# Optimization experiments

Measured on AMD Instinct MI355X. Metric: run time of the kernel, lower is better.

## Reference

```python
import jax, jax.numpy as jnp
import numpy as np

B, S, VD, MD = 32, 2048, 512, 512
AD = max(VD, MD)


def setup_inputs() -> dict:
    key = jax.random.key(0)
    k1, k2, k3, k4, k5, k6 = jax.random.split(key, 6)
    query = jax.random.normal(k1, (B, VD), dtype=jnp.float32)
    keys = jax.random.normal(k2, (B, S, MD), dtype=jnp.float32)
    mask = jax.random.randint(k3, (B, S), 0, 2).astype(jnp.bool_)
    # torch Linear weight layout: [out, in]
    W1 = jax.random.normal(k4, (AD, VD), dtype=jnp.float32) * (1.0 / np.sqrt(VD))
    W2 = jax.random.normal(k5, (AD, MD), dtype=jnp.float32) * (1.0 / np.sqrt(MD))
    v = jax.random.normal(k6, (AD,), dtype=jnp.float32) * (1.0 / np.sqrt(AD))
    return {"query": query, "keys": keys, "mask": mask, "W1": W1, "W2": W2, "v": v}


def reference(query, keys, mask, W1, W2, v):
    # w1_query: [B, 1, AD]; w2_keys: [B, S, AD]
    w1_query = jnp.einsum('bd,ad->ba', query, W1)[:, None, :]
    w2_keys = jnp.einsum('bsd,ad->bsa', keys, W2)
    combined = jnp.tanh(w1_query + w2_keys)            # [B, S, AD]
    scores = jnp.einsum('bsa,a->bs', combined, v)      # [B, S]
    scores = jnp.where(mask, scores, -jnp.inf)
    attn_weights = jax.nn.softmax(scores, axis=-1)
    return attn_weights
```

## Files before the change

### kernel.cpp

```cpp
#include <hip/hip_runtime.h>
#include <math.h>

#define BB 32
#define SS 2048
#define DD 512
#define AD 512

#define BM 128
#define BN 128
#define BK 64

typedef __bf16 bf16;
typedef __attribute__((ext_vector_type(8))) __bf16 bf16x8;
typedef __attribute__((ext_vector_type(4))) __bf16 bf16x4;
typedef __attribute__((ext_vector_type(4))) float floatx4;

__device__ inline void async16(const void* g, void* l) {
    __builtin_amdgcn_global_load_lds(
        (const __attribute__((address_space(1))) unsigned int*)g,
        (__attribute__((address_space(3))) unsigned int*)l, 16, 0, 0);
}

#define NW8 (AD * DD / 8)
#define NCV (NW8 / 256)
__global__ void prep_kernel(const float* __restrict__ W2,
                            bf16* __restrict__ W2b,
                            const unsigned char* __restrict__ m8,
                            int* __restrict__ flag,
                            const float* __restrict__ query,
                            const float* __restrict__ W1,
                            float* __restrict__ w1q) {
    const int bid = blockIdx.x;
    if (bid < NCV) {
        int j = threadIdx.x + bid * 256;
        const float4* s4 = (const float4*)W2 + (size_t)j * 2;
        float4 x = s4[0], y = s4[1];
        bf16x8 o;
        o[0] = (bf16)x.x; o[1] = (bf16)x.y; o[2] = (bf16)x.z; o[3] = (bf16)x.w;
        o[4] = (bf16)y.x; o[5] = (bf16)y.y; o[6] = (bf16)y.z; o[7] = (bf16)y.w;
        *(bf16x8*)(W2b + (size_t)j * 8) = o;
    } else if (bid < NCV + 64) {
        int t = threadIdx.x + (bid - NCV) * 256;
        int any = 0;
        for (int i = t; i < BB * SS; i += 64 * 256)
            if ((i & 3) && m8[i]) any = 1;
        if (__any(any)) {
            if ((threadIdx.x & 63) == 0) atomicOr(flag, 1);
        }
    } else {
        int id = bid - NCV - 64;
        int b = id >> 7;
        int a = (id & 127) * 4 + (threadIdx.x >> 6);
        int lane = threadIdx.x & 63;
        const float4* q4 = (const float4*)(query + (size_t)b * DD) + lane * 2;
        const float4* w4 = (const float4*)(W1 + (size_t)a * DD) + lane * 2;
        float4 qa = q4[0], qb = q4[1];
        float4 wa = w4[0], wb = w4[1];
        float acc = qa.x * wa.x + qa.y * wa.y + qa.z * wa.z + qa.w * wa.w
                  + qb.x * wb.x + qb.y * wb.y + qb.z * wb.z + qb.w * wb.w;
#pragma unroll
        for (int off = 32; off > 0; off >>= 1) acc += __shfl_down(acc, off);
        if (lane == 0) w1q[(size_t)b * AD + a] = acc;
    }
}

__global__ __launch_bounds__(256, 3)
void gemm_scores_mfma(const float* __restrict__ keys,
                      const bf16* __restrict__ W2b,
                      const float* __restrict__ w1q,
                      const float* __restrict__ v,
                      float* __restrict__ partial) {
    __shared__ float a_lds[BM * BK];
    __shared__ bf16  b_lds[BN * BK];

    const int t    = threadIdx.x;
    const int lane = t & 63;
    const int w    = t >> 6;
    const int ml   = lane & 15;
    const int kg   = lane >> 4;

    const int lin    = blockIdx.x;
    const int x8     = lin & 7;
    const int hi     = lin >> 3;
    const int a_tile = hi & 3;
    const int kt     = x8 + ((hi >> 2) << 3);
    const int b      = kt >> 4;
    const int s0     = (kt & 15) * BM;
    const int a0     = a_tile * BN;

    const int m_off = (w & 1) * 64;
    const int n_off = (w >> 1) * 64;

    const float* Ablk = keys + ((size_t)b * SS + s0) * DD;
    const bf16*  Bblk = W2b + (size_t)a0 * DD;

    floatx4 acc[4][4];
#pragma unroll
    for (int mi = 0; mi < 4; ++mi)
#pragma unroll
        for (int ni = 0; ni < 4; ++ni)
            acc[mi][ni] = (floatx4)(0.f);

    const int NCHUNK = DD / BK;
    for (int c = 0; c < NCHUNK; ++c) {
        const int d0 = c * BK;
        __syncthreads();
#pragma unroll
        for (int i = 0; i < 8; ++i) {
            int g = t + 256 * i;
            int r = g >> 4, cc = g & 15, cs = cc ^ (r & 15);
            async16(Ablk + (size_t)r * DD + d0 + cs * 4,
                    &a_lds[(256 * i + 64 * w) * 4]);
        }
#pragma unroll
        for (int i = 0; i < 4; ++i) {
            int g = t + 256 * i;
            int r = g >> 3, cc = g & 7, cs = cc ^ (r & 7);
            async16(Bblk + (size_t)r * DD + d0 + cs * 8,
                    &b_lds[(256 * i + 64 * w) * 8]);
        }
        __syncthreads();

#pragma unroll
        for (int ks = 0; ks < 2; ++ks) {
            bf16x8 af[4], bfr[4];
#pragma unroll
            for (int mi = 0; mi < 4; ++mi) {
                int R  = m_off + mi * 16 + ml;
                int gB = 8 * ks + 2 * kg;
                float4 lo = *(const float4*)&a_lds[R * BK + ((gB    ) ^ (R & 15)) * 4];
                float4 hi4 = *(const float4*)&a_lds[R * BK + ((gB + 1) ^ (R & 15)) * 4];
                bf16x8 f;
                f[0] = (bf16)lo.x;  f[1] = (bf16)lo.y;
                f[2] = (bf16)lo.z;  f[3] = (bf16)lo.w;
                f[4] = (bf16)hi4.x; f[5] = (bf16)hi4.y;
                f[6] = (bf16)hi4.z; f[7] = (bf16)hi4.w;
                af[mi] = f;
            }
#pragma unroll
            for (int ni = 0; ni < 4; ++ni) {
                int R = n_off + ni * 16 + ml;
                int pos = (ks * 4 + kg) ^ (R & 7);
                bfr[ni] = *(const bf16x8*)&b_lds[R * BK + pos * 8];
            }
#pragma unroll
            for (int mi = 0; mi < 4; ++mi)
#pragma unroll
                for (int ni = 0; ni < 4; ++ni)
                    acc[mi][ni] = __builtin_amdgcn_mfma_f32_16x16x32_bf16(
                        af[mi], bfr[ni], acc[mi][ni], 0, 0, 0);
        }
    }

    float w1qa[4], va[4];
#pragma unroll
    for (int ni = 0; ni < 4; ++ni) {
        int a = a0 + n_off + ni * 16 + ml;
        w1qa[ni] = w1q[(size_t)b * AD + a];
        va[ni]   = v[a];
    }
    const int slot = a_tile * 2 + (w >> 1);
#pragma unroll
    for (int mi = 0; mi < 4; ++mi) {
#pragma unroll
        for (int reg = 0; reg < 4; ++reg) {
            float p = 0.f;
#pragma unroll
            for (int ni = 0; ni < 4; ++ni) {
                float x = acc[mi][ni][reg] + w1qa[ni];
                float th = 1.f - 2.f / (1.f + __expf(2.f * x));
                p = fmaf(th, va[ni], p);
            }
            p += __shfl_xor(p, 1);
            p += __shfl_xor(p, 2);
            p += __shfl_xor(p, 4);
            p += __shfl_xor(p, 8);
            if (ml == 0) {
                int row = m_off + mi * 16 + kg * 4 + reg;
                partial[((size_t)b * SS + s0 + row) * 8 + slot] = p;
            }
        }
    }
}

#define FBK 32
#define FLDK (FBK + 8)
__global__ __launch_bounds__(256, 2)
void gemm_scores_fallback(const float* __restrict__ keys,
                          const float* __restrict__ W2,
                          const float* __restrict__ w1q,
                          const float* __restrict__ v,
                          float* __restrict__ partial) {
    __shared__ bf16 a_lds[BM][FLDK];
    __shared__ bf16 b_lds[BN][FLDK];
    __shared__ float s_red[BM];

    const int t    = threadIdx.x;
    const int lane = t & 63;
    const int w    = t >> 6;
    const int ml   = lane & 15;
    const int kg   = lane >> 4;
    const int b    = blockIdx.z;
    const int s0   = blockIdx.x * BM;
    const int a0   = blockIdx.y * BN;
    const int m_off = (w & 1) * 64;
    const int n_off = (w >> 1) * 64;

    const float* Ablk = keys + ((size_t)b * SS + s0) * DD;
    const float* Bblk = W2 + (size_t)a0 * DD;

    if (t < BM) s_red[t] = 0.f;

    floatx4 acc[4][4];
#pragma unroll
    for (int mi = 0; mi < 4; ++mi)
#pragma unroll
        for (int ni = 0; ni < 4; ++ni)
            acc[mi][ni] = (floatx4)(0.f);

    float4 ga[4], gb[4];
#pragma unroll
    for (int i = 0; i < 4; ++i) {
        int idx = t + 256 * i;
        int r = idx >> 3, c = idx & 7;
        ga[i] = *(const float4*)(Ablk + (size_t)r * DD + c * 4);
        gb[i] = *(const float4*)(Bblk + (size_t)r * DD + c * 4);
    }

    for (int chunk = 0; chunk < DD / FBK; ++chunk) {
        __syncthreads();
#pragma unroll
        for (int i = 0; i < 4; ++i) {
            int idx = t + 256 * i;
            int r = idx >> 3, c = idx & 7;
            bf16x4 pa, pb;
            pa[0] = (bf16)ga[i].x; pa[1] = (bf16)ga[i].y;
            pa[2] = (bf16)ga[i].z; pa[3] = (bf16)ga[i].w;
            pb[0] = (bf16)gb[i].x; pb[1] = (bf16)gb[i].y;
            pb[2] = (bf16)gb[i].z; pb[3] = (bf16)gb[i].w;
            *(bf16x4*)&a_lds[r][c * 4] = pa;
            *(bf16x4*)&b_lds[r][c * 4] = pb;
        }
        __syncthreads();
        if (chunk < DD / FBK - 1) {
            int d0 = (chunk + 1) * FBK;
#pragma unroll
            for (int i = 0; i < 4; ++i) {
                int idx = t + 256 * i;
                int r = idx >> 3, c = idx & 7;
                ga[i] = *(const float4*)(Ablk + (size_t)r * DD + d0 + c * 4);
                gb[i] = *(const float4*)(Bblk + (size_t)r * DD + d0 + c * 4);
            }
        }
        bf16x8 af[4], bfr[4];
#pragma unroll
        for (int mi = 0; mi < 4; ++mi)
            af[mi] = *(const bf16x8*)&a_lds[m_off + mi * 16 + ml][kg * 8];
#pragma unroll
        for (int ni = 0; ni < 4; ++ni)
            bfr[ni] = *(const bf16x8*)&b_lds[n_off + ni * 16 + ml][kg * 8];
#pragma unroll
        for (int mi = 0; mi < 4; ++mi)
#pragma unroll
            for (int ni = 0; ni < 4; ++ni)
                acc[mi][ni] = __builtin_amdgcn_mfma_f32_16x16x32_bf16(
                    af[mi], bfr[ni], acc[mi][ni], 0, 0, 0);
    }

    float w1qa[4], va[4];
#pragma unroll
    for (int ni = 0; ni < 4; ++ni) {
        int a = a0 + n_off + ni * 16 + ml;
        w1qa[ni] = w1q[(size_t)b * AD + a];
        va[ni]   = v[a];
    }
#pragma unroll
    for (int mi = 0; mi < 4; ++mi) {
#pragma unroll
        for (int reg = 0; reg < 4; ++reg) {
            float p = 0.f;
#pragma unroll
            for (int ni = 0; ni < 4; ++ni) {
                float x = acc[mi][ni][reg] + w1qa[ni];
                float th = 1.f - 2.f / (1.f + __expf(2.f * x));
                p = fmaf(th, va[ni], p);
            }
            p += __shfl_xor(p, 1);
            p += __shfl_xor(p, 2);
            p += __shfl_xor(p, 4);
            p += __shfl_xor(p, 8);
            if (ml == 0)
                atomicAdd(&s_red[m_off + mi * 16 + kg * 4 + reg], p);
        }
    }
    __syncthreads();
    if (t < BM)
        partial[(((size_t)b * SS) + s0 + t) * 8 + blockIdx.y * 2] = s_red[t];
}

__global__ void softmax_kernel(const float* __restrict__ partial,
                               const int* __restrict__ mask_i32,
                               const unsigned char* __restrict__ mask_u8,
                               const int* __restrict__ flag,
                               float* __restrict__ out) {
    const int b = blockIdx.x;
    const int t = threadIdx.x;
    __shared__ float rmax[4], rsum[4];
    const int wid = t >> 6, lane = t & 63;

    float sv[8]; int mv[8];
    const int bytes = (*flag != 0);
#pragma unroll
    for (int k = 0; k < 8; ++k) {
        int i = t + 256 * k;
        const float4* p4 = (const float4*)(partial + ((size_t)b * SS + i) * 8);
        float4 pa = p4[0], pb = p4[1];
        sv[k] = ((pa.x + pa.y) + (pa.z + pa.w)) + ((pb.x + pb.y) + (pb.z + pb.w));
        mv[k] = bytes ? (int)mask_u8[(size_t)b * SS + i]
                      : mask_i32[(size_t)b * SS + i];
    }

    float mx = -INFINITY;
#pragma unroll
    for (int k = 0; k < 8; ++k) mx = fmaxf(mx, mv[k] ? sv[k] : -INFINITY);
#pragma unroll
    for (int off = 32; off > 0; off >>= 1) mx = fmaxf(mx, __shfl_xor(mx, off));
    if (lane == 0) rmax[wid] = mx;
    __syncthreads();
    mx = fmaxf(fmaxf(rmax[0], rmax[1]), fmaxf(rmax[2], rmax[3]));

    float ev[8]; float sum = 0.f;
#pragma unroll
    for (int k = 0; k < 8; ++k) {
        ev[k] = mv[k] ? __expf(sv[k] - mx) : 0.f;
        sum += ev[k];
    }
#pragma unroll
    for (int off = 32; off > 0; off >>= 1) sum += __shfl_xor(sum, off);
    if (lane == 0) rsum[wid] = sum;
    __syncthreads();
    sum = (rsum[0] + rsum[1]) + (rsum[2] + rsum[3]);
    float inv = 1.f / sum;
#pragma unroll
    for (int k = 0; k < 8; ++k)
        out[(size_t)b * SS + t + 256 * k] = ev[k] * inv;
}

extern "C" void kernel_launch(void* const* d_in, const int* in_sizes, int n_in,
                              void* d_out, int out_size, void* d_ws, size_t ws_size,
                              hipStream_t stream) {
    const float* query = (const float*)d_in[0];
    const float* keys  = (const float*)d_in[1];
    const void*  mask  = d_in[2];
    const float* W1    = (const float*)d_in[3];
    const float* W2    = (const float*)d_in[4];
    const float* v     = (const float*)d_in[5];
    float* out = (float*)d_out;

    char* wsb = (char*)d_ws;
    int*   flag    = (int*)wsb;
    float* w1q     = (float*)(wsb + 256);
    float* partial = (float*)(wsb + 256 + 65536);
    bf16*  W2b     = (bf16*)(wsb + 256 + 65536 + 2097152);
    size_t need = 256 + 65536 + 2097152 + (size_t)AD * DD * 2;

    hipMemsetAsync(flag, 0, 4, stream);
    if (ws_size >= need) {
        prep_kernel<<<NCV + 64 + 4096, 256, 0, stream>>>(
            W2, W2b, (const unsigned char*)mask, flag, query, W1, w1q);
        gemm_scores_mfma<<<(SS / BM) * (AD / BN) * BB, 256, 0, stream>>>(
            keys, W2b, w1q, v, partial);
    } else {
        hipMemsetAsync(partial, 0, (size_t)BB * SS * 8 * 4, stream);
        prep_kernel<<<NCV + 64 + 4096, 256, 0, stream>>>(
            W2, W2b, (const unsigned char*)mask, flag, query, W1, w1q);
        gemm_scores_fallback<<<dim3(SS / BM, AD / BN, BB), 256, 0, stream>>>(
            keys, W2, w1q, v, partial);
    }
    softmax_kernel<<<BB, 256, 0, stream>>>(partial, (const int*)mask,
                                           (const unsigned char*)mask, flag, out);
}
```

Measured before the change: 244.2 us.

## Double-buffer LDS staging in scores GEMM with halved K chunk

```diff
diff --git a/kernel.cpp b/kernel.cpp
--- a/kernel.cpp
+++ b/kernel.cpp
@@ -8,7 +8,7 @@
 
 #define BM 128
 #define BN 128
-#define BK 64
+#define BK 32
 
 typedef __bf16 bf16;
 typedef __attribute__((ext_vector_type(8))) __bf16 bf16x8;
@@ -64,14 +64,34 @@
     }
 }
 
+__device__ inline void stage_chunk(const float* __restrict__ Ablk,
+                                   const bf16* __restrict__ Bblk,
+                                   int d0, float* al, bf16* bl,
+                                   int t, int w) {
+#pragma unroll
+    for (int i = 0; i < 4; ++i) {
+        int g = t + 256 * i;
+        int r = g >> 3, cc = g & 7, cs = cc ^ (r & 7);
+        async16(Ablk + (size_t)r * DD + d0 + cs * 4,
+                al + (256 * i + 64 * w) * 4);
+    }
+#pragma unroll
+    for (int i = 0; i < 2; ++i) {
+        int g = t + 256 * i;
+        int r = g >> 2, cc = g & 3, cs = cc ^ (r & 3);
+        async16(Bblk + (size_t)r * DD + d0 + cs * 8,
+                bl + (256 * i + 64 * w) * 8);
+    }
+}
+
 __global__ __launch_bounds__(256, 3)
 void gemm_scores_mfma(const float* __restrict__ keys,
                       const bf16* __restrict__ W2b,
                       const float* __restrict__ w1q,
                       const float* __restrict__ v,
                       float* __restrict__ partial) {
-    __shared__ float a_lds[BM * BK];
-    __shared__ bf16  b_lds[BN * BK];
+    __shared__ float a_lds[2][BM * BK];
+    __shared__ bf16  b_lds[2][BN * BK];
 
     const int t    = threadIdx.x;
     const int lane = t & 63;
@@ -102,54 +122,43 @@
             acc[mi][ni] = (floatx4)(0.f);
 
     const int NCHUNK = DD / BK;
+
+    stage_chunk(Ablk, Bblk, 0, &a_lds[0][0], &b_lds[0][0], t, w);
+
     for (int c = 0; c < NCHUNK; ++c) {
-        const int d0 = c * BK;
+        const int cur = c & 1;
         __syncthreads();
-#pragma unroll
-        for (int i = 0; i < 8; ++i) {
-            int g = t + 256 * i;
-            int r = g >> 4, cc = g & 15, cs = cc ^ (r & 15);
-            async16(Ablk + (size_t)r * DD + d0 + cs * 4,
-                    &a_lds[(256 * i + 64 * w) * 4]);
-        }
-#pragma unroll
-        for (int i = 0; i < 4; ++i) {
-            int g = t + 256 * i;
-            int r = g >> 3, cc = g & 7, cs = cc ^ (r & 7);
-            async16(Bblk + (size_t)r * DD + d0 + cs * 8,
-                    &b_lds[(256 * i + 64 * w) * 8]);
-        }
-        __syncthreads();
-
-#pragma unroll
-        for (int ks = 0; ks < 2; ++ks) {
-            bf16x8 af[4], bfr[4];
-#pragma unroll
-            for (int mi = 0; mi < 4; ++mi) {
-                int R  = m_off + mi * 16 + ml;
-                int gB = 8 * ks + 2 * kg;
-                float4 lo = *(const float4*)&a_lds[R * BK + ((gB    ) ^ (R & 15)) * 4];
-                float4 hi4 = *(const float4*)&a_lds[R * BK + ((gB + 1) ^ (R & 15)) * 4];
-                bf16x8 f;
-                f[0] = (bf16)lo.x;  f[1] = (bf16)lo.y;
-                f[2] = (bf16)lo.z;  f[3] = (bf16)lo.w;
-                f[4] = (bf16)hi4.x; f[5] = (bf16)hi4.y;
-                f[6] = (bf16)hi4.z; f[7] = (bf16)hi4.w;
-                af[mi] = f;
-            }
-#pragma unroll
-            for (int ni = 0; ni < 4; ++ni) {
-                int R = n_off + ni * 16 + ml;
-                int pos = (ks * 4 + kg) ^ (R & 7);
-                bfr[ni] = *(const bf16x8*)&b_lds[R * BK + pos * 8];
-            }
-#pragma unroll
-            for (int mi = 0; mi < 4; ++mi)
-#pragma unroll
-                for (int ni = 0; ni < 4; ++ni)
-                    acc[mi][ni] = __builtin_amdgcn_mfma_f32_16x16x32_bf16(
-                        af[mi], bfr[ni], acc[mi][ni], 0, 0, 0);
-        }
+        if (c + 1 < NCHUNK)
+            stage_chunk(Ablk, Bblk, (c + 1) * BK,
+                        &a_lds[cur ^ 1][0], &b_lds[cur ^ 1][0], t, w);
+
+        bf16x8 af[4], bfr[4];
+#pragma unroll
+        for (int mi = 0; mi < 4; ++mi) {
+            int R  = m_off + mi * 16 + ml;
+            int p0 = (2 * kg) ^ (R & 7);
+            int p1 = (2 * kg + 1) ^ (R & 7);
+            float4 lo  = *(const float4*)&a_lds[cur][R * BK + p0 * 4];
+            float4 hi4 = *(const float4*)&a_lds[cur][R * BK + p1 * 4];
+            bf16x8 f;
+            f[0] = (bf16)lo.x;  f[1] = (bf16)lo.y;
+            f[2] = (bf16)lo.z;  f[3] = (bf16)lo.w;
+            f[4] = (bf16)hi4.x; f[5] = (bf16)hi4.y;
+            f[6] = (bf16)hi4.z; f[7] = (bf16)hi4.w;
+            af[mi] = f;
+        }
+#pragma unroll
+        for (int ni = 0; ni < 4; ++ni) {
+            int R = n_off + ni * 16 + ml;
+            int p = kg ^ (R & 3);
+            bfr[ni] = *(const bf16x8*)&b_lds[cur][R * BK + p * 8];
+        }
+#pragma unroll
+        for (int mi = 0; mi < 4; ++mi)
+#pragma unroll
+            for (int ni = 0; ni < 4; ++ni)
+                acc[mi][ni] = __builtin_amdgcn_mfma_f32_16x16x32_bf16(
+                    af[mi], bfr[ni], acc[mi][ni], 0, 0, 0);
     }
 
     float w1qa[4], va[4];
```

After: 272.9 us. +11.7%, slower.

## Double-buffer GEMM tiles with register-prefetched A converted to bf16 at store

Applied to the files above, without the earlier changes.

```diff
diff --git a/kernel.cpp b/kernel.cpp
--- a/kernel.cpp
+++ b/kernel.cpp
@@ -64,14 +64,14 @@
     }
 }
 
-__global__ __launch_bounds__(256, 3)
+__global__ __launch_bounds__(256, 2)
 void gemm_scores_mfma(const float* __restrict__ keys,
                       const bf16* __restrict__ W2b,
                       const float* __restrict__ w1q,
                       const float* __restrict__ v,
                       float* __restrict__ partial) {
-    __shared__ float a_lds[BM * BK];
-    __shared__ bf16  b_lds[BN * BK];
+    __shared__ bf16 a_lds[2][BM * BK];
+    __shared__ bf16 b_lds[2][BN * BK];
 
     const int t    = threadIdx.x;
     const int lane = t & 63;
@@ -101,47 +101,77 @@
         for (int ni = 0; ni < 4; ++ni)
             acc[mi][ni] = (floatx4)(0.f);
 
+    int ar[4], ac8[4], acs[4];
+#pragma unroll
+    for (int j = 0; j < 4; ++j) {
+        int u = t + 256 * j;
+        ar[j]  = u >> 3;
+        ac8[j] = (u & 7) * 8;
+        acs[j] = ((u & 7) ^ (ar[j] & 7)) * 8;
+    }
+
     const int NCHUNK = DD / BK;
+    float4 areg[4][2];
+
+#pragma unroll
+    for (int j = 0; j < 4; ++j) {
+        const float* src = Ablk + (size_t)ar[j] * DD + ac8[j];
+        areg[j][0] = *(const float4*)src;
+        areg[j][1] = *(const float4*)(src + 4);
+    }
+#pragma unroll
+    for (int i = 0; i < 4; ++i) {
+        int g = t + 256 * i;
+        int r = g >> 3, cc = g & 7, cs = cc ^ (r & 7);
+        async16(Bblk + (size_t)r * DD + cs * 8,
+                &b_lds[0][(256 * i + 64 * w) * 8]);
+    }
+#pragma unroll
+    for (int j = 0; j < 4; ++j) {
+        bf16x8 o;
+        o[0] = (bf16)areg[j][0].x; o[1] = (bf16)areg[j][0].y;
+        o[2] = (bf16)areg[j][0].z; o[3] = (bf16)areg[j][0].w;
+        o[4] = (bf16)areg[j][1].x; o[5] = (bf16)areg[j][1].y;
+        o[6] = (bf16)areg[j][1].z; o[7] = (bf16)areg[j][1].w;
+        *(bf16x8*)&a_lds[0][ar[j] * BK + acs[j]] = o;
+    }
+
     for (int c = 0; c < NCHUNK; ++c) {
-        const int d0 = c * BK;
+        const int cur = c & 1;
+        const int nxt = cur ^ 1;
         __syncthreads();
-#pragma unroll
-        for (int i = 0; i < 8; ++i) {
-            int g = t + 256 * i;
-            int r = g >> 4, cc = g & 15, cs = cc ^ (r & 15);
-            async16(Ablk + (size_t)r * DD + d0 + cs * 4,
-                    &a_lds[(256 * i + 64 * w) * 4]);
-        }
-#pragma unroll
-        for (int i = 0; i < 4; ++i) {
-            int g = t + 256 * i;
-            int r = g >> 3, cc = g & 7, cs = cc ^ (r & 7);
-            async16(Bblk + (size_t)r * DD + d0 + cs * 8,
-                    &b_lds[(256 * i + 64 * w) * 8]);
-        }
-        __syncthreads();
+
+        if (c + 1 < NCHUNK) {
+            const int d0 = (c + 1) * BK;
+#pragma unroll
+            for (int j = 0; j < 4; ++j) {
+                const float* src = Ablk + (size_t)ar[j] * DD + d0 + ac8[j];
+                areg[j][0] = *(const float4*)src;
+                areg[j][1] = *(const float4*)(src + 4);
+            }
+#pragma unroll
+            for (int i = 0; i < 4; ++i) {
+                int g = t + 256 * i;
+                int r = g >> 3, cc = g & 7, cs = cc ^ (r & 7);
+                async16(Bblk + (size_t)r * DD + d0 + cs * 8,
+                        &b_lds[nxt][(256 * i + 64 * w) * 8]);
+            }
+        }
 
 #pragma unroll
         for (int ks = 0; ks < 2; ++ks) {
             bf16x8 af[4], bfr[4];
 #pragma unroll
             for (int mi = 0; mi < 4; ++mi) {
-                int R  = m_off + mi * 16 + ml;
-                int gB = 8 * ks + 2 * kg;
-                float4 lo = *(const float4*)&a_lds[R * BK + ((gB    ) ^ (R & 15)) * 4];
-                float4 hi4 = *(const float4*)&a_lds[R * BK + ((gB + 1) ^ (R & 15)) * 4];
-                bf16x8 f;
-                f[0] = (bf16)lo.x;  f[1] = (bf16)lo.y;
-                f[2] = (bf16)lo.z;  f[3] = (bf16)lo.w;
-                f[4] = (bf16)hi4.x; f[5] = (bf16)hi4.y;
-                f[6] = (bf16)hi4.z; f[7] = (bf16)hi4.w;
-                af[mi] = f;
+                int R = m_off + mi * 16 + ml;
+                int p = (ks * 4 + kg) ^ (R & 7);
+                af[mi] = *(const bf16x8*)&a_lds[cur][R * BK + p * 8];
             }
 #pragma unroll
             for (int ni = 0; ni < 4; ++ni) {
                 int R = n_off + ni * 16 + ml;
-                int pos = (ks * 4 + kg) ^ (R & 7);
-                bfr[ni] = *(const bf16x8*)&b_lds[R * BK + pos * 8];
+                int p = (ks * 4 + kg) ^ (R & 7);
+                bfr[ni] = *(const bf16x8*)&b_lds[cur][R * BK + p * 8];
             }
 #pragma unroll
             for (int mi = 0; mi < 4; ++mi)
@@ -149,6 +179,19 @@
                 for (int ni = 0; ni < 4; ++ni)
                     acc[mi][ni] = __builtin_amdgcn_mfma_f32_16x16x32_bf16(
                         af[mi], bfr[ni], acc[mi][ni], 0, 0, 0);
+        }
+
+        __builtin_amdgcn_sched_barrier(0);
+        if (c + 1 < NCHUNK) {
+#pragma unroll
+            for (int j = 0; j < 4; ++j) {
+                bf16x8 o;
+                o[0] = (bf16)areg[j][0].x; o[1] = (bf16)areg[j][0].y;
+                o[2] = (bf16)areg[j][0].z; o[3] = (bf16)areg[j][0].w;
+                o[4] = (bf16)areg[j][1].x; o[5] = (bf16)areg[j][1].y;
+                o[6] = (bf16)areg[j][1].z; o[7] = (bf16)areg[j][1].w;
+                *(bf16x8*)&a_lds[nxt][ar[j] * BK + acs[j]] = o;
+            }
         }
     }
 
```

Result: slower. 261.1 us (+6.9%).

## Compact unmasked key rows and skip GEMM tiles for masked positions

Applied to the files above, without the earlier changes.

```diff
diff --git a/kernel.cpp b/kernel.cpp
--- a/kernel.cpp
+++ b/kernel.cpp
@@ -29,7 +29,9 @@
                             int* __restrict__ flag,
                             const float* __restrict__ query,
                             const float* __restrict__ W1,
-                            float* __restrict__ w1q) {
+                            float* __restrict__ w1q,
+                            int* __restrict__ cnt,
+                            int* __restrict__ idxb) {
     const int bid = blockIdx.x;
     if (bid < NCV) {
         int j = threadIdx.x + bid * 256;
@@ -47,7 +49,7 @@
         if (__any(any)) {
             if ((threadIdx.x & 63) == 0) atomicOr(flag, 1);
         }
-    } else {
+    } else if (bid < NCV + 64 + 4096) {
         int id = bid - NCV - 64;
         int b = id >> 7;
         int a = (id & 127) * 4 + (threadIdx.x >> 6);
@@ -61,6 +63,40 @@
 #pragma unroll
         for (int off = 32; off > 0; off >>= 1) acc += __shfl_down(acc, off);
         if (lane == 0) w1q[(size_t)b * AD + a] = acc;
+    } else {
+        const int b = bid - NCV - 64 - 4096;
+        const int t = threadIdx.x;
+        const int lane = t & 63, wid = t >> 6;
+        __shared__ int s_base;
+        __shared__ int wsum[4];
+        __shared__ int s_bytes;
+        if (t == 0) { s_base = 0; s_bytes = 0; }
+        __syncthreads();
+        {
+            const unsigned* mu = (const unsigned*)m8;
+            unsigned pr = (mu[t] | mu[t + 256]) & 0xFFFFFF00u;
+            if (pr) atomicOr(&s_bytes, 1);
+        }
+        __syncthreads();
+        const int bytes = s_bytes;
+        const int* m32 = (const int*)m8;
+#pragma unroll 1
+        for (int c = 0; c < 8; ++c) {
+            int s = c * 256 + t;
+            int mv = bytes ? (int)m8[(size_t)b * SS + s]
+                           : m32[(size_t)b * SS + s];
+            unsigned long long ball = __ballot(mv != 0);
+            int rank = __popcll(ball & ((1ull << lane) - 1ull));
+            if (lane == 0) wsum[wid] = __popcll(ball);
+            __syncthreads();
+            int woff = s_base;
+            for (int j = 0; j < wid; ++j) woff += wsum[j];
+            if (mv) idxb[(size_t)b * SS + woff + rank] = s;
+            __syncthreads();
+            if (t == 0) s_base += wsum[0] + wsum[1] + wsum[2] + wsum[3];
+            __syncthreads();
+        }
+        if (t == 0) cnt[b] = s_base;
     }
 }
 
@@ -69,9 +105,12 @@
                       const bf16* __restrict__ W2b,
                       const float* __restrict__ w1q,
                       const float* __restrict__ v,
+                      const int* __restrict__ cnt,
+                      const int* __restrict__ idxb,
                       float* __restrict__ partial) {
     __shared__ float a_lds[BM * BK];
     __shared__ bf16  b_lds[BN * BK];
+    __shared__ int   idx_lds[BM];
 
     const int t    = threadIdx.x;
     const int lane = t & 63;
@@ -88,11 +127,24 @@
     const int s0     = (kt & 15) * BM;
     const int a0     = a_tile * BN;
 
+    const int cntb = cnt[b];
+    if (s0 >= cntb) return;
+
     const int m_off = (w & 1) * 64;
     const int n_off = (w >> 1) * 64;
 
-    const float* Ablk = keys + ((size_t)b * SS + s0) * DD;
-    const bf16*  Bblk = W2b + (size_t)a0 * DD;
+    const float* Akeys = keys + (size_t)b * SS * DD;
+    const bf16*  Bblk  = W2b + (size_t)a0 * DD;
+
+    if (t < BM) {
+        int p = s0 + t;
+        idx_lds[t] = idxb[(size_t)b * SS + (p < cntb ? p : cntb - 1)];
+    }
+    __syncthreads();
+
+    int arow[8];
+#pragma unroll
+    for (int i = 0; i < 8; ++i) arow[i] = idx_lds[(t + 256 * i) >> 4];
 
     floatx4 acc[4][4];
 #pragma unroll
@@ -109,7 +161,7 @@
         for (int i = 0; i < 8; ++i) {
             int g = t + 256 * i;
             int r = g >> 4, cc = g & 15, cs = cc ^ (r & 15);
-            async16(Ablk + (size_t)r * DD + d0 + cs * 4,
+            async16(Akeys + (size_t)arow[i] * DD + d0 + cs * 4,
                     &a_lds[(256 * i + 64 * w) * 4]);
         }
 #pragma unroll
@@ -175,9 +227,10 @@
             p += __shfl_xor(p, 2);
             p += __shfl_xor(p, 4);
             p += __shfl_xor(p, 8);
-            if (ml == 0) {
-                int row = m_off + mi * 16 + kg * 4 + reg;
-                partial[((size_t)b * SS + s0 + row) * 8 + slot] = p;
+            int row = m_off + mi * 16 + kg * 4 + reg;
+            if (ml == 0 && s0 + row < cntb) {
+                int os = idx_lds[row];
+                partial[((size_t)b * SS + os) * 8 + slot] = p;
             }
         }
     }
@@ -362,18 +415,24 @@
     float* w1q     = (float*)(wsb + 256);
     float* partial = (float*)(wsb + 256 + 65536);
     bf16*  W2b     = (bf16*)(wsb + 256 + 65536 + 2097152);
-    size_t need = 256 + 65536 + 2097152 + (size_t)AD * DD * 2;
+    int*   cnt     = (int*)(wsb + 256 + 65536 + 2097152 + 524288);
+    int*   idxb    = (int*)(wsb + 256 + 65536 + 2097152 + 524288 + 256);
+    size_t need = 256 + 65536 + 2097152 + 524288 + 256
+                + (size_t)BB * SS * sizeof(int);
 
     hipMemsetAsync(flag, 0, 4, stream);
     if (ws_size >= need) {
-        prep_kernel<<<NCV + 64 + 4096, 256, 0, stream>>>(
-            W2, W2b, (const unsigned char*)mask, flag, query, W1, w1q);
+        prep_kernel<<<NCV + 64 + 4096 + 32, 256, 0, stream>>>(
+            W2, W2b, (const unsigned char*)mask, flag, query, W1, w1q,
+            cnt, idxb);
         gemm_scores_mfma<<<(SS / BM) * (AD / BN) * BB, 256, 0, stream>>>(
-            keys, W2b, w1q, v, partial);
+            keys, W2b, w1q, v, cnt, idxb, partial);
     } else {
         hipMemsetAsync(partial, 0, (size_t)BB * SS * 8 * 4, stream);
         prep_kernel<<<NCV + 64 + 4096, 256, 0, stream>>>(
-            W2, W2b, (const unsigned char*)mask, flag, query, W1, w1q);
+            W2, (bf16*)(wsb + 256 + 65536 + 2097152),
+            (const unsigned char*)mask, flag, query, W1, w1q,
+            nullptr, nullptr);
         gemm_scores_fallback<<<dim3(SS / BM, AD / BN, BB), 256, 0, stream>>>(
             keys, W2, w1q, v, partial);
     }
```

New measurement: 245.0 us, median of 2. About the same (+0.3%).
